# Optimization experiments

Hardware: AMD Instinct MI355X
Metric: run time of the kernel (lower is better)

## Reference

```python
import math
import jax, jax.numpy as jnp
import numpy as np

PATCH_NUMS = (1, 2, 3, 4, 5, 6, 8, 10, 13, 16)
_lens = [p * p for p in PATCH_NUMS]
_cum = np.concatenate([[0], np.cumsum(_lens)])
BEGIN_ENDS = [(int(_cum[i]), int(_cum[i + 1])) for i in range(len(PATCH_NUMS))]
L_TOTAL = int(_cum[-1])  # 680

B, C = 32, 1024
S, P, M, R, NCAT = 10, 8, 4, 8, 22
SLOTS = P * M  # 32 slots per scale
MEM_RANK = 64
ALPHA_HID = 128


def setup_inputs() -> dict:
    key = jax.random.key(0)
    ks = jax.random.split(key, 24)
    inp = {}
    inp['x'] = jax.random.normal(ks[0], (B, L_TOTAL, C), jnp.float32)
    # -1 means CFG-unconditional sample (no category memory)
    inp['category_ids'] = jax.random.randint(ks[1], (B,), -1, NCAT)
    # shared memory, orthogonal-ish init rescaled to xavier std sqrt(2/(C+C))
    inp['shared_memory'] = jax.random.normal(ks[2], (S, SLOTS, C)) * math.sqrt(1.0 / C)
    inp['cat_A'] = jax.random.normal(ks[3], (NCAT, S, R)) * 0.01
    inp['cat_B'] = jax.random.normal(ks[4], (S, R, SLOTS * C)) * (1.0 / math.sqrt(R))
    inp['cat_emb'] = jax.random.normal(ks[5], (NCAT, C)) * 0.02
    inp['scale_emb'] = jax.random.normal(ks[6], (S, C)) * 0.02
    inp['Wq'] = jax.random.normal(ks[7], (C, C)) * (1.0 / math.sqrt(C))
    inp['Wk'] = jax.random.normal(ks[8], (C, C)) * (1.0 / math.sqrt(C))
    inp['Wv'] = jax.random.normal(ks[9], (C, C)) * (1.0 / math.sqrt(C))
    inp['aW1'] = jax.random.normal(ks[10], (3 * C, ALPHA_HID)) * (1.0 / math.sqrt(3 * C))
    inp['ab1'] = jnp.zeros((ALPHA_HID,), jnp.float32)
    inp['aW2'] = jax.random.normal(ks[11], (ALPHA_HID, 1)) * 0.01  # init zeros in torch; small random to exercise math
    inp['ab2'] = jnp.full((1,), -1.0, jnp.float32)
    inp['kW1'] = jax.random.normal(ks[12], (C, MEM_RANK)) * (1.0 / math.sqrt(C))
    inp['kb1'] = jnp.zeros((MEM_RANK,), jnp.float32)
    inp['kW2'] = jax.random.normal(ks[13], (MEM_RANK, C)) * (1.0 / math.sqrt(MEM_RANK))
    inp['kb2'] = jnp.zeros((C,), jnp.float32)
    inp['vW1'] = jax.random.normal(ks[14], (C, MEM_RANK)) * (1.0 / math.sqrt(C))
    inp['vb1'] = jnp.zeros((MEM_RANK,), jnp.float32)
    inp['vW2'] = jax.random.normal(ks[15], (MEM_RANK, C)) * (1.0 / math.sqrt(MEM_RANK))
    inp['vb2'] = jnp.zeros((C,), jnp.float32)
    inp['gk_logit'] = jnp.float32(-2.0)  # block_idx=0, depth=16
    inp['gv_logit'] = jnp.float32(-2.0)
    inp['log_temp'] = jnp.float32(math.log(0.1))
    return inp


def reference(x, category_ids, shared_memory, cat_A, cat_B, cat_emb, scale_emb,
              Wq, Wk, Wv, aW1, ab1, aW2, ab2,
              kW1, kb1, kW2, kb2, vW1, vb1, vW2, vb2,
              gk_logit, gv_logit, log_temp):
    Bb, L, Cc = x.shape
    temp = jnp.clip(jnp.exp(log_temp), 0.05, 1.0)
    inv_sqrt_c = 1.0 / math.sqrt(Cc)

    query = x @ Wq                              # [B, L, C]
    shared_k = shared_memory @ Wk               # [S, slots, C]
    shared_v = shared_memory @ Wv

    valid = (category_ids >= 0)                 # [B]
    cid = jnp.clip(category_ids, 0, None)
    a_all = cat_A[cid]                          # [B, S, R]
    ce = cat_emb[cid]                           # [B, C]

    outs = []
    for i, (s, e) in enumerate(BEGIN_ENDS):
        q = query[:, s:e, :]                    # [B, Ls, C]
        Ls = e - s
        V = i + 1                               # visible scales
        # --- shared retrieval over visible slots ---
        ks_ = shared_k[:V].reshape(V * SLOTS, Cc)
        vs_ = shared_v[:V].reshape(V * SLOTS, Cc)
        attn_s = jax.nn.softmax((q @ ks_.T) * inv_sqrt_c / temp, axis=-1)
        o_s = attn_s @ vs_                      # [B, Ls, C]
        # --- per-category memory: shared + low-rank residual ---
        delta = jnp.einsum('bvr,vrd->bvd', a_all[:, :V], cat_B[:V])
        delta = delta.reshape(Bb, V, SLOTS, Cc)
        cat_mem = (shared_memory[:V][None] + delta).reshape(Bb, V * SLOTS, Cc)
        kc = cat_mem @ Wk                       # [B, Vs, C]
        vc = cat_mem @ Wv
        attn_c = jax.nn.softmax(jnp.einsum('bld,bsd->bls', q, kc) * inv_sqrt_c / temp, axis=-1)
        o_c = jnp.einsum('bls,bsd->bld', attn_c, vc)
        # --- learned alpha blend (zeroed for invalid / CFG categories) ---
        ai = jnp.concatenate([
            q,
            jnp.broadcast_to(ce[:, None, :], (Bb, Ls, Cc)),
            jnp.broadcast_to(scale_emb[i][None, None, :], (Bb, Ls, Cc)),
        ], axis=-1)                             # [B, Ls, 3C]
        h = jax.nn.gelu(ai @ aW1 + ab1, approximate=False)
        alpha = jax.nn.sigmoid(h @ aW2 + ab2)   # [B, Ls, 1]
        alpha = jnp.where(valid[:, None, None], alpha, 0.0)
        outs.append(o_s + alpha * (o_c - o_s))

    mem = jnp.concatenate(outs, axis=1)         # [B, L, C]
    mem_k = jax.nn.sigmoid(gk_logit) * ((mem @ kW1 + kb1) @ kW2 + kb2)
    mem_v = jax.nn.sigmoid(gv_logit) * ((mem @ vW1 + vb1) @ vW2 + vb2)
    zero = jnp.float32(0.0)
    return mem_k, mem_v, zero, zero
```

## Files before the change

### kernel.cpp

```cpp
#include <hip/hip_runtime.h>
#include <math.h>

#define NB 32
#define NC 1024
#define LTOT 680

typedef unsigned short u16;
typedef __bf16 bf16x8 __attribute__((ext_vector_type(8)));
typedef float floatx4 __attribute__((ext_vector_type(4)));

__device__ __forceinline__ u16 f2bf(float f)
{
    union { float f; unsigned u; } v; v.f = f;
    unsigned u = v.u;
    u += 0x7FFFu + ((u >> 16) & 1u);
    return (u16)(u >> 16);
}

__device__ __forceinline__ float bf2f(unsigned u)
{
    union { unsigned u; float f; } v; v.u = u << 16; return v.f;
}

template<int AFP32, int OUTBF>
__global__ __launch_bounds__(256) void gemm_mfma(
    const void* __restrict__ Av, const u16* __restrict__ BT,
    float* __restrict__ C, int M, int N, int K, int lda,
    const float* __restrict__ bias, const float* __restrict__ scale_logit)
{
    __shared__ __align__(16) u16 As[16 * 64 * 8];
    __shared__ __align__(16) u16 Bs[16 * 64 * 8];

    const int tid  = threadIdx.x;
    const int m0   = blockIdx.x << 7;
    const int n0   = blockIdx.y << 7;
    const int wave = tid >> 6;
    const int lane = tid & 63;
    const int mh   = wave & 1;
    const int nh   = wave >> 1;

    floatx4 acc[4][4];
#pragma unroll
    for (int i = 0; i < 4; ++i)
#pragma unroll
        for (int j = 0; j < 4; ++j) acc[i][j] = (floatx4){0.f, 0.f, 0.f, 0.f};

    for (int k0 = 0; k0 < K; k0 += 64) {
        __syncthreads();
        if (AFP32) {
            const float* A = (const float*)Av;
#pragma unroll
            for (int p = 0; p < 8; ++p) {
                int q   = tid + (p << 8);
                int row = q >> 4;
                int fq  = q & 15;
                int gr  = m0 + row; if (gr > M - 1) gr = M - 1;
                const float4 a4 = *(const float4*)(A + (size_t)gr * lda + k0 + (fq << 2));
                int kh = fq >> 3, quad = (fq >> 1) & 3, jh = fq & 1;
                u16* d = &As[((((row >> 4) << 1) | kh) * 64 + (quad << 4) + (row & 15)) * 8 + (jh << 2)];
                d[0] = f2bf(a4.x); d[1] = f2bf(a4.y); d[2] = f2bf(a4.z); d[3] = f2bf(a4.w);
            }
        } else {
            const u16* A = (const u16*)Av;
#pragma unroll
            for (int p = 0; p < 4; ++p) {
                int q   = tid + (p << 8);
                int row = q >> 3;
                int cq  = q & 7;
                int gr  = m0 + row; if (gr > M - 1) gr = M - 1;
                *(uint4*)&As[((((row >> 4) << 1) | (cq >> 2)) * 64 + ((cq & 3) << 4) + (row & 15)) * 8]
                    = *(const uint4*)(A + (size_t)gr * lda + k0 + (cq << 3));
            }
        }
#pragma unroll
        for (int p = 0; p < 4; ++p) {
            int q   = tid + (p << 8);
            int row = q >> 3;
            int cq  = q & 7;
            int gn  = n0 + row; if (gn > N - 1) gn = N - 1;
            *(uint4*)&Bs[((((row >> 4) << 1) | (cq >> 2)) * 64 + ((cq & 3) << 4) + (row & 15)) * 8]
                = *(const uint4*)(BT + (size_t)gn * K + k0 + (cq << 3));
        }
        __syncthreads();
#pragma unroll
        for (int kh = 0; kh < 2; ++kh) {
            bf16x8 a[4], b[4];
#pragma unroll
            for (int i = 0; i < 4; ++i)
                a[i] = *(const bf16x8*)&As[(((((mh << 2) + i) << 1) | kh) * 64 + lane) * 8];
#pragma unroll
            for (int j = 0; j < 4; ++j)
                b[j] = *(const bf16x8*)&Bs[(((((nh << 2) + j) << 1) | kh) * 64 + lane) * 8];
#pragma unroll
            for (int i = 0; i < 4; ++i)
#pragma unroll
                for (int j = 0; j < 4; ++j)
                    acc[i][j] = __builtin_amdgcn_mfma_f32_16x16x32_bf16(a[i], b[j], acc[i][j], 0, 0, 0);
        }
    }

    float scale = 1.f;
    if (scale_logit) scale = 1.f / (1.f + __expf(-scale_logit[0]));
    const int col = lane & 15, rquad = lane >> 4;
#pragma unroll
    for (int i = 0; i < 4; ++i) {
#pragma unroll
        for (int j = 0; j < 4; ++j) {
#pragma unroll
            for (int r = 0; r < 4; ++r) {
                int gr = m0 + (mh << 6) + (i << 4) + (rquad << 2) + r;
                int gc = n0 + (nh << 6) + (j << 4) + col;
                if (gr < M && gc < N) {
                    float bb = bias ? bias[gc] : 0.f;
                    float val = scale * (acc[i][j][r] + bb);
                    if (OUTBF) ((u16*)C)[(size_t)gr * N + gc] = f2bf(val);
                    else       C[(size_t)gr * N + gc] = val;
                }
            }
        }
    }
}

__global__ __launch_bounds__(256) void gemm_logits(
    const u16* __restrict__ Q, const u16* __restrict__ skb,
    const u16* __restrict__ kcb, float* __restrict__ out)
{
    __shared__ __align__(16) u16 As[16 * 64 * 8];
    __shared__ __align__(16) u16 Bs[16 * 64 * 8];

    const int tid  = threadIdx.x;
    const int m0   = blockIdx.x << 7;
    const int n0   = blockIdx.y << 7;
    const int b    = blockIdx.z;
    const int wave = tid >> 6;
    const int lane = tid & 63;
    const int mh   = wave & 1;
    const int nh   = wave >> 1;

    const u16* Ab = Q   + (size_t)b * 680 * 1024;
    const u16* KC = kcb + (size_t)b * 320 * 1024;

    floatx4 acc[4][4];
#pragma unroll
    for (int i = 0; i < 4; ++i)
#pragma unroll
        for (int j = 0; j < 4; ++j) acc[i][j] = (floatx4){0.f, 0.f, 0.f, 0.f};

    for (int k0 = 0; k0 < 1024; k0 += 64) {
        __syncthreads();
#pragma unroll
        for (int p = 0; p < 4; ++p) {
            int q = tid + (p << 8);
            int row = q >> 3, cq = q & 7;
            int gr = m0 + row; if (gr > 679) gr = 679;
            *(uint4*)&As[((((row >> 4) << 1) | (cq >> 2)) * 64 + ((cq & 3) << 4) + (row & 15)) * 8]
                = *(const uint4*)(Ab + (size_t)gr * 1024 + k0 + (cq << 3));
        }
#pragma unroll
        for (int p = 0; p < 4; ++p) {
            int q = tid + (p << 8);
            int row = q >> 3, cq = q & 7;
            int gn = n0 + row;
            const u16* src = (gn < 320) ? (skb + (size_t)gn * 1024)
                                        : (KC + (size_t)(gn - 320) * 1024);
            *(uint4*)&Bs[((((row >> 4) << 1) | (cq >> 2)) * 64 + ((cq & 3) << 4) + (row & 15)) * 8]
                = *(const uint4*)(src + k0 + (cq << 3));
        }
        __syncthreads();
#pragma unroll
        for (int kh = 0; kh < 2; ++kh) {
            bf16x8 a[4], bb[4];
#pragma unroll
            for (int i = 0; i < 4; ++i)
                a[i] = *(const bf16x8*)&As[(((((mh << 2) + i) << 1) | kh) * 64 + lane) * 8];
#pragma unroll
            for (int j = 0; j < 4; ++j)
                bb[j] = *(const bf16x8*)&Bs[(((((nh << 2) + j) << 1) | kh) * 64 + lane) * 8];
#pragma unroll
            for (int i = 0; i < 4; ++i)
#pragma unroll
                for (int j = 0; j < 4; ++j)
                    acc[i][j] = __builtin_amdgcn_mfma_f32_16x16x32_bf16(a[i], bb[j], acc[i][j], 0, 0, 0);
        }
    }

    const int col = lane & 15, rquad = lane >> 4;
#pragma unroll
    for (int i = 0; i < 4; ++i)
#pragma unroll
        for (int j = 0; j < 4; ++j)
#pragma unroll
            for (int r = 0; r < 4; ++r) {
                int gr = m0 + (mh << 6) + (i << 4) + (rquad << 2) + r;
                int gc = n0 + (nh << 6) + (j << 4) + col;
                if (gr < 680)
                    out[((size_t)b * 680 + gr) * 640 + gc] = acc[i][j][r];
            }
}

__global__ __launch_bounds__(256) void gemm_pv(
    const u16* __restrict__ P, const u16* __restrict__ svT,
    const u16* __restrict__ vcT, float* __restrict__ out)
{
    __shared__ __align__(16) u16 As[16 * 64 * 8];
    __shared__ __align__(16) u16 Bs[16 * 64 * 8];

    const int tid  = threadIdx.x;
    const int m0   = blockIdx.x << 7;
    const int n0   = blockIdx.y << 7;
    const int b    = blockIdx.z;
    const int wave = tid >> 6;
    const int lane = tid & 63;
    const int mh   = wave & 1;
    const int nh   = wave >> 1;

    floatx4 acc[4][4];
#pragma unroll
    for (int i = 0; i < 4; ++i)
#pragma unroll
        for (int j = 0; j < 4; ++j) acc[i][j] = (floatx4){0.f, 0.f, 0.f, 0.f};

    for (int k0 = 0; k0 < 640; k0 += 64) {
        __syncthreads();
#pragma unroll
        for (int p = 0; p < 4; ++p) {
            int q = tid + (p << 8);
            int row = q >> 3, cq = q & 7;
            int gr = m0 + row; if (gr > 679) gr = 679;
            *(uint4*)&As[((((row >> 4) << 1) | (cq >> 2)) * 64 + ((cq & 3) << 4) + (row & 15)) * 8]
                = *(const uint4*)(P + ((size_t)b * 680 + gr) * 1280 + k0 + (cq << 3));
        }
#pragma unroll
        for (int p = 0; p < 4; ++p) {
            int q = tid + (p << 8);
            int row = q >> 3, cq = q & 7;
            int gn = n0 + row;
            const u16* src = (k0 < 320)
                ? (svT + (size_t)gn * 320 + k0)
                : (vcT + ((size_t)b * 1024 + gn) * 320 + (k0 - 320));
            *(uint4*)&Bs[((((row >> 4) << 1) | (cq >> 2)) * 64 + ((cq & 3) << 4) + (row & 15)) * 8]
                = *(const uint4*)(src + (cq << 3));
        }
        __syncthreads();
#pragma unroll
        for (int kh = 0; kh < 2; ++kh) {
            bf16x8 a[4], bb[4];
#pragma unroll
            for (int i = 0; i < 4; ++i)
                a[i] = *(const bf16x8*)&As[(((((mh << 2) + i) << 1) | kh) * 64 + lane) * 8];
#pragma unroll
            for (int j = 0; j < 4; ++j)
                bb[j] = *(const bf16x8*)&Bs[(((((nh << 2) + j) << 1) | kh) * 64 + lane) * 8];
#pragma unroll
            for (int i = 0; i < 4; ++i)
#pragma unroll
                for (int j = 0; j < 4; ++j)
                    acc[i][j] = __builtin_amdgcn_mfma_f32_16x16x32_bf16(a[i], bb[j], acc[i][j], 0, 0, 0);
        }
    }

    const int col = lane & 15, rquad = lane >> 4;
#pragma unroll
    for (int i = 0; i < 4; ++i)
#pragma unroll
        for (int j = 0; j < 4; ++j)
#pragma unroll
            for (int r = 0; r < 4; ++r) {
                int gr = m0 + (mh << 6) + (i << 4) + (rquad << 2) + r;
                int gc = n0 + (nh << 6) + (j << 4) + col;
                if (gr < 680)
                    out[((size_t)b * 680 + gr) * 1024 + gc] = acc[i][j][r];
            }
}

__global__ __launch_bounds__(256) void gemm_halpha(
    const u16* __restrict__ Q, const u16* __restrict__ W,
    const float* __restrict__ ceW, const float* __restrict__ seW,
    const int* __restrict__ cat_ids, u16* __restrict__ h)
{
    __shared__ __align__(16) u16 As[16 * 64 * 8];
    __shared__ __align__(16) u16 Bs[16 * 64 * 8];

    const int tid  = threadIdx.x;
    const int m0   = blockIdx.x << 7;
    const int wave = tid >> 6;
    const int lane = tid & 63;
    const int mh   = wave & 1;
    const int nh   = wave >> 1;

    floatx4 acc[4][4];
#pragma unroll
    for (int i = 0; i < 4; ++i)
#pragma unroll
        for (int j = 0; j < 4; ++j) acc[i][j] = (floatx4){0.f, 0.f, 0.f, 0.f};

    for (int k0 = 0; k0 < 1024; k0 += 64) {
        __syncthreads();
#pragma unroll
        for (int p = 0; p < 4; ++p) {
            int q = tid + (p << 8);
            int row = q >> 3, cq = q & 7;
            int gr = m0 + row;
            *(uint4*)&As[((((row >> 4) << 1) | (cq >> 2)) * 64 + ((cq & 3) << 4) + (row & 15)) * 8]
                = *(const uint4*)(Q + (size_t)gr * 1024 + k0 + (cq << 3));
        }
#pragma unroll
        for (int p = 0; p < 4; ++p) {
            int q = tid + (p << 8);
            int row = q >> 3, cq = q & 7;
            *(uint4*)&Bs[((((row >> 4) << 1) | (cq >> 2)) * 64 + ((cq & 3) << 4) + (row & 15)) * 8]
                = *(const uint4*)(W + (size_t)row * 1024 + k0 + (cq << 3));
        }
        __syncthreads();
#pragma unroll
        for (int kh = 0; kh < 2; ++kh) {
            bf16x8 a[4], bb[4];
#pragma unroll
            for (int i = 0; i < 4; ++i)
                a[i] = *(const bf16x8*)&As[(((((mh << 2) + i) << 1) | kh) * 64 + lane) * 8];
#pragma unroll
            for (int j = 0; j < 4; ++j)
                bb[j] = *(const bf16x8*)&Bs[(((((nh << 2) + j) << 1) | kh) * 64 + lane) * 8];
#pragma unroll
            for (int i = 0; i < 4; ++i)
#pragma unroll
                for (int j = 0; j < 4; ++j)
                    acc[i][j] = __builtin_amdgcn_mfma_f32_16x16x32_bf16(a[i], bb[j], acc[i][j], 0, 0, 0);
        }
    }

    const int se_[9] = {1,5,14,30,55,91,155,255,424};
    const int col = lane & 15, rquad = lane >> 4;
#pragma unroll
    for (int i = 0; i < 4; ++i) {
#pragma unroll
        for (int r = 0; r < 4; ++r) {
            int gr = m0 + (mh << 6) + (i << 4) + (rquad << 2) + r;
            int b  = gr / 680;
            int l  = gr - b * 680;
            int isc = 0;
#pragma unroll
            for (int k = 0; k < 9; ++k) if (l >= se_[k]) isc = k + 1;
            int cid = cat_ids[b]; if (cid < 0) cid = 0;
            const float* cw = ceW + cid * 128;
            const float* sw = seW + isc * 128;
#pragma unroll
            for (int j = 0; j < 4; ++j) {
                int gc = (nh << 6) + (j << 4) + col;
                float val = acc[i][j][r] + cw[gc] + sw[gc];
                float g = 0.5f * val * (1.0f + erff(val * 0.70710678118654752f));
                h[(size_t)gr * 128 + gc] = f2bf(g);
            }
        }
    }
}

__global__ __launch_bounds__(256) void alpha_reduce(
    const u16* __restrict__ h, const float* __restrict__ aW2,
    const float* __restrict__ ab2, const int* __restrict__ cat_ids,
    float* __restrict__ alpha)
{
    const int wave = threadIdx.x >> 6;
    const int lane = threadIdx.x & 63;
    const int row  = (blockIdx.x << 2) + wave;

    const unsigned pk = *(const unsigned*)(h + (size_t)row * 128 + (lane << 1));
    float s = bf2f(pk) * aW2[lane << 1] + bf2f(pk >> 16) * aW2[(lane << 1) + 1];
#pragma unroll
    for (int k = 32; k >= 1; k >>= 1) s += __shfl_xor(s, k);
    if (lane == 0) {
        int b = row / 680;
        float al = 0.f;
        if (cat_ids[b] >= 0) al = 1.f / (1.f + expf(-(s + ab2[0])));
        alpha[row] = al;
    }
}

__global__ __launch_bounds__(256) void softmax_kernel(
    float* __restrict__ logits, const float* __restrict__ alpha,
    const float* __restrict__ log_temp)
{
    const int tid  = threadIdx.x;
    const int w    = tid >> 6;
    const int lane = tid & 63;
    const int b    = blockIdx.y;
    const int l    = (blockIdx.x << 2) + w;

    const int se[10] = {1,5,14,30,55,91,155,255,424,680};
    int isc = 0;
#pragma unroll
    for (int k = 0; k < 9; ++k) if (l >= se[k]) isc = k + 1;
    const int NK = (isc + 1) << 5;

    float temp = __expf(log_temp[0]);
    temp = fminf(fmaxf(temp, 0.05f), 1.0f);
    const float Ksc = 0.03125f / temp;

    float* row = logits + ((size_t)b * 680 + l) * 640;

    float ls[5], lc[5];
#pragma unroll
    for (int u = 0; u < 5; ++u) {
        int j = lane + (u << 6);
        bool v = j < NK;
        ls[u] = v ? row[j]       : -1e30f;
        lc[u] = v ? row[320 + j] : -1e30f;
    }
    float mxs = -1e30f, mxc = -1e30f;
#pragma unroll
    for (int u = 0; u < 5; ++u) { mxs = fmaxf(mxs, ls[u]); mxc = fmaxf(mxc, lc[u]); }
#pragma unroll
    for (int k = 32; k >= 1; k >>= 1) {
        mxs = fmaxf(mxs, __shfl_xor(mxs, k));
        mxc = fmaxf(mxc, __shfl_xor(mxc, k));
    }
    float es[5], ec[5], ss = 0.f, sc = 0.f;
#pragma unroll
    for (int u = 0; u < 5; ++u) {
        int j = lane + (u << 6);
        bool v = j < NK;
        es[u] = v ? __expf((ls[u] - mxs) * Ksc) : 0.f;
        ec[u] = v ? __expf((lc[u] - mxc) * Ksc) : 0.f;
        ss += es[u]; sc += ec[u];
    }
#pragma unroll
    for (int k = 32; k >= 1; k >>= 1) {
        ss += __shfl_xor(ss, k);
        sc += __shfl_xor(sc, k);
    }
    const float al = alpha[b * LTOT + l];
    const float wS = (1.f - al) / ss;
    const float wC = al / sc;

    u16* po = (u16*)row;
#pragma unroll
    for (int u = 0; u < 5; ++u) {
        int j = lane + (u << 6);
        po[j]       = f2bf(es[u] * wS);
        po[320 + j] = f2bf(ec[u] * wC);
    }
}

__global__ __launch_bounds__(256) void castbf(
    const float* __restrict__ in, u16* __restrict__ out, int n4)
{
    int i = blockIdx.x * 256 + threadIdx.x;
    const int stride = gridDim.x * 256;
    for (; i < n4; i += stride) {
        const float4 v = ((const float4*)in)[i];
        uint2 o;
        o.x = (unsigned)f2bf(v.x) | ((unsigned)f2bf(v.y) << 16);
        o.y = (unsigned)f2bf(v.z) | ((unsigned)f2bf(v.w) << 16);
        ((uint2*)out)[i] = o;
    }
}

__global__ __launch_bounds__(256) void tcast(
    const float* __restrict__ in, u16* __restrict__ out, int R, int Cc)
{
    __shared__ float t[32][33];
    const int bx = blockIdx.x * 32;
    const int by = blockIdx.y * 32;
    const int x = threadIdx.x & 31;
    const int y0 = threadIdx.x >> 5;
#pragma unroll
    for (int yy = y0; yy < 32; yy += 8)
        t[yy][x] = (by + yy < R && bx + x < Cc)
                 ? in[(size_t)(by + yy) * Cc + bx + x] : 0.f;
    __syncthreads();
#pragma unroll
    for (int yy = y0; yy < 32; yy += 8)
        if (bx + yy < Cc && by + x < R)
            out[(size_t)(bx + yy) * R + by + x] = f2bf(t[x][yy]);
}

__global__ __launch_bounds__(256) void transpose32(
    const float* __restrict__ in, float* __restrict__ out, int R, int Cc)
{
    __shared__ float t[32][33];
    const int bx = blockIdx.x * 32;
    const int by = blockIdx.y * 32;
    const int x = threadIdx.x & 31;
    const int y0 = threadIdx.x >> 5;
#pragma unroll
    for (int yy = y0; yy < 32; yy += 8)
        t[yy][x] = (by + yy < R && bx + x < Cc)
                 ? in[(size_t)(by + yy) * Cc + bx + x] : 0.f;
    __syncthreads();
#pragma unroll
    for (int yy = y0; yy < 32; yy += 8)
        if (bx + yy < Cc && by + x < R)
            out[(size_t)(bx + yy) * R + by + x] = t[x][yy];
}

__global__ __launch_bounds__(256) void build_kc(
    const float* __restrict__ sk, const float* __restrict__ catBK,
    const float* __restrict__ cat_A, const int* __restrict__ cat_ids,
    u16* __restrict__ kc)
{
    const int b = blockIdx.x;
    const int jrow = blockIdx.y;
    const int v = jrow >> 5, slot = jrow & 31;
    int cid = cat_ids[b]; if (cid < 0) cid = 0;
    float a[8];
#pragma unroll
    for (int r = 0; r < 8; ++r) a[r] = cat_A[(cid * 10 + v) * 8 + r];
    const int c = threadIdx.x << 2;
    float4 acc = *(const float4*)(sk + (size_t)jrow * 1024 + c);
#pragma unroll
    for (int r = 0; r < 8; ++r) {
        const float4 bv = *(const float4*)(catBK + (size_t)((v * 8 + r) * 32 + slot) * 1024 + c);
        acc.x = fmaf(a[r], bv.x, acc.x);
        acc.y = fmaf(a[r], bv.y, acc.y);
        acc.z = fmaf(a[r], bv.z, acc.z);
        acc.w = fmaf(a[r], bv.w, acc.w);
    }
    uint2 pk;
    pk.x = (unsigned)f2bf(acc.x) | ((unsigned)f2bf(acc.y) << 16);
    pk.y = (unsigned)f2bf(acc.z) | ((unsigned)f2bf(acc.w) << 16);
    *(uint2*)(kc + ((size_t)b * 320 + jrow) * 1024 + c) = pk;
}

__global__ __launch_bounds__(320) void build_vcT(
    const float* __restrict__ svT, const float* __restrict__ catBVT,
    const float* __restrict__ cat_A, const int* __restrict__ cat_ids,
    u16* __restrict__ vcT)
{
    __shared__ float aS[80];
    const int b = blockIdx.x;
    const int c = blockIdx.y;
    const int tid = threadIdx.x;
    if (tid < 80) {
        int cid = cat_ids[b]; if (cid < 0) cid = 0;
        aS[tid] = cat_A[cid * 80 + tid];
    }
    __syncthreads();
    const int j = tid;
    const int v = j >> 5, slot = j & 31;
    float acc = svT[(size_t)c * 320 + j];
    const float* row = catBVT + (size_t)c * 2560;
#pragma unroll
    for (int r = 0; r < 8; ++r)
        acc = fmaf(aS[v * 8 + r], row[(v * 8 + r) * 32 + slot], acc);
    vcT[((size_t)b * 1024 + c) * 320 + j] = f2bf(acc);
}

__global__ void concat_bias(const float* __restrict__ a,
                            const float* __restrict__ b, float* __restrict__ o)
{
    int t = threadIdx.x;
    if (t < 64) o[t] = a[t];
    else if (t < 128) o[t] = b[t - 64];
}

__global__ void tail_zero(float* p)
{
    if (threadIdx.x < 2) p[threadIdx.x] = 0.f;
}

extern "C" void kernel_launch(void* const* d_in, const int* in_sizes, int n_in,
                              void* d_out, int out_size, void* d_ws, size_t ws_size,
                              hipStream_t stream)
{
    (void)in_sizes; (void)n_in;
    const float* x         = (const float*)d_in[0];
    const int*   cat_ids   = (const int*)  d_in[1];
    const float* sm        = (const float*)d_in[2];
    const float* cat_A     = (const float*)d_in[3];
    const float* cat_B     = (const float*)d_in[4];
    const float* cat_emb   = (const float*)d_in[5];
    const float* scale_emb = (const float*)d_in[6];
    const float* Wq        = (const float*)d_in[7];
    const float* Wk        = (const float*)d_in[8];
    const float* Wv        = (const float*)d_in[9];
    const float* aW1       = (const float*)d_in[10];
    const float* ab1       = (const float*)d_in[11];
    const float* aW2       = (const float*)d_in[12];
    const float* ab2       = (const float*)d_in[13];
    const float* kW1       = (const float*)d_in[14];
    const float* kb1       = (const float*)d_in[15];
    const float* kW2       = (const float*)d_in[16];
    const float* kb2       = (const float*)d_in[17];
    const float* vW1       = (const float*)d_in[18];
    const float* vb1       = (const float*)d_in[19];
    const float* vW2       = (const float*)d_in[20];
    const float* vb2       = (const float*)d_in[21];
    const float* gk        = (const float*)d_in[22];
    const float* gv        = (const float*)d_in[23];
    const float* log_temp  = (const float*)d_in[24];

    float* out   = (float*)d_out;
    float* memb  = out;
    float* outv  = out + (size_t)21760 * 1024;

    float* w      = (float*)d_ws;
    u16*   kc_bf  = (u16*)w;
    u16*   vcT_bf = (u16*)(w + 5242880);
    float* sk     = w + 10485760;
    float* sv     = w + 10813440;
    float* svT    = w + 11141120;
    u16*   sk_bf  = (u16*)(w + 11468800);
    u16*   svT_bf = (u16*)(w + 11632640);
    float* alph   = w + 11796480;
    float* logits = w + 11859200;
    float* tail0  = w + 25785600;
    u16*   aW1topT = (u16*)tail0;
    u16*   aW1midT = (u16*)(tail0 + 65536);
    u16*   aW1botT = (u16*)(tail0 + 131072);
    float* ceW    = tail0 + 196608;
    float* seW    = tail0 + 199424;
    float* cb     = tail0 + 200704;
    u16*   h_bf   = (u16*)(tail0 + 200832);
    if (ws_size < (size_t)29881600 * 4) return;
    if (out_size < 2 * 21760 * 1024 + 2) return;

    u16*   x_bf   = (u16*)logits;
    float* bufA   = logits + 5570560;
    float* bufB   = bufA + 2621440;
    float* catBVT = bufB + 2621440;
    u16*   WqT    = (u16*)w;
    u16*   WkT    = WqT + 1048576;
    u16*   WvT    = WkT + 1048576;
    u16*   kW1T   = (u16*)sv;
    u16*   vW1T   = kW1T + 65536;
    u16*   kW2T   = vW1T + 65536;
    u16*   vW2T   = kW2T + 65536;
    float* bufAB  = w;
    u16*   query_bf = (u16*)outv;

    const dim3 blk256(256);

    castbf<<<dim3(2048), blk256, 0, stream>>>(x, x_bf, 21760 * 1024 / 4);
    tcast<<<dim3(32, 32), blk256, 0, stream>>>(Wq, WqT, 1024, 1024);
    tcast<<<dim3(32, 32), blk256, 0, stream>>>(Wk, WkT, 1024, 1024);
    tcast<<<dim3(32, 32), blk256, 0, stream>>>(Wv, WvT, 1024, 1024);
    tcast<<<dim3(4, 32), blk256, 0, stream>>>(aW1,              aW1topT, 1024, 128);
    tcast<<<dim3(4, 32), blk256, 0, stream>>>(aW1 + 1024 * 128, aW1midT, 1024, 128);
    tcast<<<dim3(4, 32), blk256, 0, stream>>>(aW1 + 2048 * 128, aW1botT, 1024, 128);

    gemm_mfma<0,1><<<dim3(170, 8), blk256, 0, stream>>>(x_bf, WqT, (float*)query_bf, 21760, 1024, 1024, 1024, nullptr, nullptr);
    gemm_mfma<1,0><<<dim3(3, 8),   blk256, 0, stream>>>(sm,   WkT, sk,   320,  1024, 1024, 1024, nullptr, nullptr);
    gemm_mfma<1,0><<<dim3(3, 8),   blk256, 0, stream>>>(sm,   WvT, sv,   320,  1024, 1024, 1024, nullptr, nullptr);
    gemm_mfma<1,0><<<dim3(20, 8),  blk256, 0, stream>>>(cat_B, WkT, bufA, 2560, 1024, 1024, 1024, nullptr, nullptr);
    gemm_mfma<1,0><<<dim3(20, 8),  blk256, 0, stream>>>(cat_B, WvT, bufB, 2560, 1024, 1024, 1024, nullptr, nullptr);

    gemm_mfma<1,0><<<dim3(1, 1), blk256, 0, stream>>>(cat_emb,   aW1midT, ceW, 22, 128, 1024, 1024, nullptr, nullptr);
    gemm_mfma<1,0><<<dim3(1, 1), blk256, 0, stream>>>(scale_emb, aW1botT, seW, 10, 128, 1024, 1024, ab1, nullptr);

    castbf<<<dim3(320), blk256, 0, stream>>>(sk, sk_bf, 320 * 1024 / 4);
    transpose32<<<dim3(32, 10), blk256, 0, stream>>>(sv, svT, 320, 1024);
    tcast<<<dim3(32, 10), blk256, 0, stream>>>(sv, svT_bf, 320, 1024);
    transpose32<<<dim3(32, 80), blk256, 0, stream>>>(bufB, catBVT, 2560, 1024);
    tcast<<<dim3(2, 32), blk256, 0, stream>>>(kW1, kW1T, 1024, 64);
    tcast<<<dim3(2, 32), blk256, 0, stream>>>(vW1, vW1T, 1024, 64);
    tcast<<<dim3(32, 2), blk256, 0, stream>>>(kW2, kW2T, 64, 1024);
    tcast<<<dim3(32, 2), blk256, 0, stream>>>(vW2, vW2T, 64, 1024);
    concat_bias<<<dim3(1), dim3(128), 0, stream>>>(kb1, vb1, cb);

    build_kc<<<dim3(NB, 320), blk256, 0, stream>>>(sk, bufA, cat_A, cat_ids, kc_bf);
    build_vcT<<<dim3(NB, 1024), dim3(320), 0, stream>>>(svT, catBVT, cat_A, cat_ids, vcT_bf);

    gemm_halpha<<<dim3(170), blk256, 0, stream>>>(query_bf, aW1topT, ceW, seW, cat_ids, h_bf);
    alpha_reduce<<<dim3(5440), blk256, 0, stream>>>(h_bf, aW2, ab2, cat_ids, alph);

    gemm_logits<<<dim3(6, 5, NB), blk256, 0, stream>>>(query_bf, sk_bf, kc_bf, logits);
    softmax_kernel<<<dim3(170, NB), blk256, 0, stream>>>(logits, alph, log_temp);
    gemm_pv<<<dim3(6, 8, NB), blk256, 0, stream>>>((const u16*)logits, svT_bf, vcT_bf, memb);

    gemm_mfma<1,0><<<dim3(170, 1), blk256, 0, stream>>>(memb, kW1T, bufAB, 21760, 128, 1024, 1024, cb, nullptr);
    gemm_mfma<1,0><<<dim3(170, 8), blk256, 0, stream>>>(bufAB,      kW2T, memb, 21760, 1024, 64, 128, kb2, gk);
    gemm_mfma<1,0><<<dim3(170, 8), blk256, 0, stream>>>(bufAB + 64, vW2T, outv, 21760, 1024, 64, 128, vb2, gv);

    tail_zero<<<1, 64, 0, stream>>>(out + (size_t)2 * 21760 * 1024);
}
```

Baseline: 1.101 ms.

## Use direct global-to-LDS loads and bf16 intermediates across GEMM kernels

Swaps register-staged global loads into shared memory for the gfx9 global_load_lds path in every bf16 GEMM kernel, with per-thread source pointers precomputed once. To make more GEMMs take the bf16 path, it pre-casts shared_memory and cat_B to bf16 and makes the PV output and low-rank intermediate bf16 instead of fp32. It also swaps the grid axes so N tiles vary fastest, improving reuse of A tiles in cache. This cuts LDS store instructions and fp32 traffic, at the cost of extra cast kernels and reduced precision in intermediates.

```diff
diff --git a/kernel.cpp b/kernel.cpp
--- a/kernel.cpp
+++ b/kernel.cpp
@@ -20,6 +20,22 @@
 __device__ __forceinline__ float bf2f(unsigned u)
 {
     union { unsigned u; float f; } v; v.u = u << 16; return v.f;
+}
+
+__device__ __forceinline__ void gload16(const u16* g, u16* l)
+{
+    typedef __attribute__((address_space(1))) const void gv_t;
+    typedef __attribute__((address_space(3))) void lv_t;
+    __builtin_amdgcn_global_load_lds(
+        (gv_t*)(unsigned long long)(const void*)g,
+        (lv_t*)(unsigned int)(unsigned long long)(void*)l,
+        16, 0, 0);
+}
+
+__device__ __forceinline__ void slot_decode(int s, int* prow, int* pcq)
+{
+    *prow = ((s >> 7) << 4) | (s & 15);
+    *pcq  = (((s >> 6) & 1) << 2) | ((s >> 4) & 3);
 }
 
 template<int AFP32, int OUTBF>
@@ -32,12 +48,27 @@
     __shared__ __align__(16) u16 Bs[16 * 64 * 8];
 
     const int tid  = threadIdx.x;
-    const int m0   = blockIdx.x << 7;
-    const int n0   = blockIdx.y << 7;
+    const int m0   = blockIdx.y << 7;
+    const int n0   = blockIdx.x << 7;
     const int wave = tid >> 6;
     const int lane = tid & 63;
     const int mh   = wave & 1;
     const int nh   = wave >> 1;
+
+    const u16* aSrc[4];
+    const u16* bSrc[4];
+#pragma unroll
+    for (int p = 0; p < 4; ++p) {
+        int s, row, cq;
+        s = tid + (p << 8);
+        slot_decode(s, &row, &cq);
+        if (!AFP32) {
+            int gr = m0 + row; if (gr > M - 1) gr = M - 1;
+            aSrc[p] = (const u16*)Av + (size_t)gr * lda + (cq << 3);
+        }
+        int gn = n0 + row; if (gn > N - 1) gn = N - 1;
+        bSrc[p] = BT + (size_t)gn * K + (cq << 3);
+    }
 
     floatx4 acc[4][4];
 #pragma unroll
@@ -61,26 +92,13 @@
                 d[0] = f2bf(a4.x); d[1] = f2bf(a4.y); d[2] = f2bf(a4.z); d[3] = f2bf(a4.w);
             }
         } else {
-            const u16* A = (const u16*)Av;
-#pragma unroll
-            for (int p = 0; p < 4; ++p) {
-                int q   = tid + (p << 8);
-                int row = q >> 3;
-                int cq  = q & 7;
-                int gr  = m0 + row; if (gr > M - 1) gr = M - 1;
-                *(uint4*)&As[((((row >> 4) << 1) | (cq >> 2)) * 64 + ((cq & 3) << 4) + (row & 15)) * 8]
-                    = *(const uint4*)(A + (size_t)gr * lda + k0 + (cq << 3));
-            }
-        }
-#pragma unroll
-        for (int p = 0; p < 4; ++p) {
-            int q   = tid + (p << 8);
-            int row = q >> 3;
-            int cq  = q & 7;
-            int gn  = n0 + row; if (gn > N - 1) gn = N - 1;
-            *(uint4*)&Bs[((((row >> 4) << 1) | (cq >> 2)) * 64 + ((cq & 3) << 4) + (row & 15)) * 8]
-                = *(const uint4*)(BT + (size_t)gn * K + k0 + (cq << 3));
-        }
+#pragma unroll
+            for (int p = 0; p < 4; ++p)
+                gload16(aSrc[p] + k0, As + ((wave << 6) + (p << 8)) * 8);
+        }
+#pragma unroll
+        for (int p = 0; p < 4; ++p)
+            gload16(bSrc[p] + k0, Bs + ((wave << 6) + (p << 8)) * 8);
         __syncthreads();
 #pragma unroll
         for (int kh = 0; kh < 2; ++kh) {
@@ -140,6 +158,20 @@
     const u16* Ab = Q   + (size_t)b * 680 * 1024;
     const u16* KC = kcb + (size_t)b * 320 * 1024;
 
+    const u16* aSrc[4];
+    const u16* bSrc[4];
+#pragma unroll
+    for (int p = 0; p < 4; ++p) {
+        int s, row, cq;
+        s = tid + (p << 8);
+        slot_decode(s, &row, &cq);
+        int gr = m0 + row; if (gr > 679) gr = 679;
+        aSrc[p] = Ab + (size_t)gr * 1024 + (cq << 3);
+        int gn = n0 + row;
+        bSrc[p] = ((gn < 320) ? (skb + (size_t)gn * 1024)
+                              : (KC + (size_t)(gn - 320) * 1024)) + (cq << 3);
+    }
+
     floatx4 acc[4][4];
 #pragma unroll
     for (int i = 0; i < 4; ++i)
@@ -149,23 +181,11 @@
     for (int k0 = 0; k0 < 1024; k0 += 64) {
         __syncthreads();
 #pragma unroll
-        for (int p = 0; p < 4; ++p) {
-            int q = tid + (p << 8);
-            int row = q >> 3, cq = q & 7;
-            int gr = m0 + row; if (gr > 679) gr = 679;
-            *(uint4*)&As[((((row >> 4) << 1) | (cq >> 2)) * 64 + ((cq & 3) << 4) + (row & 15)) * 8]
-                = *(const uint4*)(Ab + (size_t)gr * 1024 + k0 + (cq << 3));
-        }
-#pragma unroll
-        for (int p = 0; p < 4; ++p) {
-            int q = tid + (p << 8);
-            int row = q >> 3, cq = q & 7;
-            int gn = n0 + row;
-            const u16* src = (gn < 320) ? (skb + (size_t)gn * 1024)
-                                        : (KC + (size_t)(gn - 320) * 1024);
-            *(uint4*)&Bs[((((row >> 4) << 1) | (cq >> 2)) * 64 + ((cq & 3) << 4) + (row & 15)) * 8]
-                = *(const uint4*)(src + k0 + (cq << 3));
-        }
+        for (int p = 0; p < 4; ++p)
+            gload16(aSrc[p] + k0, As + ((wave << 6) + (p << 8)) * 8);
+#pragma unroll
+        for (int p = 0; p < 4; ++p)
+            gload16(bSrc[p] + k0, Bs + ((wave << 6) + (p << 8)) * 8);
         __syncthreads();
 #pragma unroll
         for (int kh = 0; kh < 2; ++kh) {
@@ -200,7 +220,7 @@
 
 __global__ __launch_bounds__(256) void gemm_pv(
     const u16* __restrict__ P, const u16* __restrict__ svT,
-    const u16* __restrict__ vcT, float* __restrict__ out)
+    const u16* __restrict__ vcT, u16* __restrict__ out)
 {
     __shared__ __align__(16) u16 As[16 * 64 * 8];
     __shared__ __align__(16) u16 Bs[16 * 64 * 8];
@@ -214,6 +234,21 @@
     const int mh   = wave & 1;
     const int nh   = wave >> 1;
 
+    const u16* aSrc[4];
+    const u16* bSrcS[4];
+    const u16* bSrcC[4];
+#pragma unroll
+    for (int p = 0; p < 4; ++p) {
+        int s, row, cq;
+        s = tid + (p << 8);
+        slot_decode(s, &row, &cq);
+        int gr = m0 + row; if (gr > 679) gr = 679;
+        aSrc[p] = P + ((size_t)b * 680 + gr) * 1280 + (cq << 3);
+        int gn = n0 + row;
+        bSrcS[p] = svT + (size_t)gn * 320 + (cq << 3);
+        bSrcC[p] = vcT + ((size_t)b * 1024 + gn) * 320 + (cq << 3);
+    }
+
     floatx4 acc[4][4];
 #pragma unroll
     for (int i = 0; i < 4; ++i)
@@ -223,23 +258,12 @@
     for (int k0 = 0; k0 < 640; k0 += 64) {
         __syncthreads();
 #pragma unroll
+        for (int p = 0; p < 4; ++p)
+            gload16(aSrc[p] + k0, As + ((wave << 6) + (p << 8)) * 8);
+#pragma unroll
         for (int p = 0; p < 4; ++p) {
-            int q = tid + (p << 8);
-            int row = q >> 3, cq = q & 7;
-            int gr = m0 + row; if (gr > 679) gr = 679;
-            *(uint4*)&As[((((row >> 4) << 1) | (cq >> 2)) * 64 + ((cq & 3) << 4) + (row & 15)) * 8]
-                = *(const uint4*)(P + ((size_t)b * 680 + gr) * 1280 + k0 + (cq << 3));
-        }
-#pragma unroll
-        for (int p = 0; p < 4; ++p) {
-            int q = tid + (p << 8);
-            int row = q >> 3, cq = q & 7;
-            int gn = n0 + row;
-            const u16* src = (k0 < 320)
-                ? (svT + (size_t)gn * 320 + k0)
-                : (vcT + ((size_t)b * 1024 + gn) * 320 + (k0 - 320));
-            *(uint4*)&Bs[((((row >> 4) << 1) | (cq >> 2)) * 64 + ((cq & 3) << 4) + (row & 15)) * 8]
-                = *(const uint4*)(src + (cq << 3));
+            const u16* bp = (k0 < 320) ? (bSrcS[p] + k0) : (bSrcC[p] + (k0 - 320));
+            gload16(bp, Bs + ((wave << 6) + (p << 8)) * 8);
         }
         __syncthreads();
 #pragma unroll
@@ -269,7 +293,7 @@
                 int gr = m0 + (mh << 6) + (i << 4) + (rquad << 2) + r;
                 int gc = n0 + (nh << 6) + (j << 4) + col;
                 if (gr < 680)
-                    out[((size_t)b * 680 + gr) * 1024 + gc] = acc[i][j][r];
+                    out[((size_t)b * 680 + gr) * 1024 + gc] = f2bf(acc[i][j][r]);
             }
 }
 
@@ -288,6 +312,17 @@
     const int mh   = wave & 1;
     const int nh   = wave >> 1;
 
+    const u16* aSrc[4];
+    const u16* bSrc[4];
+#pragma unroll
+    for (int p = 0; p < 4; ++p) {
+        int s, row, cq;
+        s = tid + (p << 8);
+        slot_decode(s, &row, &cq);
+        aSrc[p] = Q + (size_t)(m0 + row) * 1024 + (cq << 3);
+        bSrc[p] = W + (size_t)row * 1024 + (cq << 3);
+    }
+
     floatx4 acc[4][4];
 #pragma unroll
     for (int i = 0; i < 4; ++i)
@@ -297,20 +332,11 @@
     for (int k0 = 0; k0 < 1024; k0 += 64) {
         __syncthreads();
 #pragma unroll
-        for (int p = 0; p < 4; ++p) {
-            int q = tid + (p << 8);
-            int row = q >> 3, cq = q & 7;
-            int gr = m0 + row;
-            *(uint4*)&As[((((row >> 4) << 1) | (cq >> 2)) * 64 + ((cq & 3) << 4) + (row & 15)) * 8]
-                = *(const uint4*)(Q + (size_t)gr * 1024 + k0 + (cq << 3));
-        }
-#pragma unroll
-        for (int p = 0; p < 4; ++p) {
-            int q = tid + (p << 8);
-            int row = q >> 3, cq = q & 7;
-            *(uint4*)&Bs[((((row >> 4) << 1) | (cq >> 2)) * 64 + ((cq & 3) << 4) + (row & 15)) * 8]
-                = *(const uint4*)(W + (size_t)row * 1024 + k0 + (cq << 3));
-        }
+        for (int p = 0; p < 4; ++p)
+            gload16(aSrc[p] + k0, As + ((wave << 6) + (p << 8)) * 8);
+#pragma unroll
+        for (int p = 0; p < 4; ++p)
+            gload16(bSrc[p] + k0, Bs + ((wave << 6) + (p << 8)) * 8);
         __syncthreads();
 #pragma unroll
         for (int kh = 0; kh < 2; ++kh) {
@@ -611,6 +637,8 @@
     float* seW    = tail0 + 199424;
     float* cb     = tail0 + 200704;
     u16*   h_bf   = (u16*)(tail0 + 200832);
+    u16*   catB_bf = (u16*)(w + 27379072);
+    u16*   sm_bf  = (u16*)(w + 28689792);
     if (ws_size < (size_t)29881600 * 4) return;
     if (out_size < 2 * 21760 * 1024 + 2) return;
 
@@ -625,12 +653,15 @@
     u16*   vW1T   = kW1T + 65536;
     u16*   kW2T   = vW1T + 65536;
     u16*   vW2T   = kW2T + 65536;
-    float* bufAB  = w;
+    u16*   bufAB_bf = (u16*)w;
+    u16*   mem_bf = (u16*)memb;
     u16*   query_bf = (u16*)outv;
 
     const dim3 blk256(256);
 
     castbf<<<dim3(2048), blk256, 0, stream>>>(x, x_bf, 21760 * 1024 / 4);
+    castbf<<<dim3(320), blk256, 0, stream>>>(sm, sm_bf, 320 * 1024 / 4);
+    castbf<<<dim3(2048), blk256, 0, stream>>>(cat_B, catB_bf, 2560 * 1024 / 4);
     tcast<<<dim3(32, 32), blk256, 0, stream>>>(Wq, WqT, 1024, 1024);
     tcast<<<dim3(32, 32), blk256, 0, stream>>>(Wk, WkT, 1024, 1024);
     tcast<<<dim3(32, 32), blk256, 0, stream>>>(Wv, WvT, 1024, 1024);
@@ -638,11 +669,11 @@
     tcast<<<dim3(4, 32), blk256, 0, stream>>>(aW1 + 1024 * 128, aW1midT, 1024, 128);
     tcast<<<dim3(4, 32), blk256, 0, stream>>>(aW1 + 2048 * 128, aW1botT, 1024, 128);
 
-    gemm_mfma<0,1><<<dim3(170, 8), blk256, 0, stream>>>(x_bf, WqT, (float*)query_bf, 21760, 1024, 1024, 1024, nullptr, nullptr);
-    gemm_mfma<1,0><<<dim3(3, 8),   blk256, 0, stream>>>(sm,   WkT, sk,   320,  1024, 1024, 1024, nullptr, nullptr);
-    gemm_mfma<1,0><<<dim3(3, 8),   blk256, 0, stream>>>(sm,   WvT, sv,   320,  1024, 1024, 1024, nullptr, nullptr);
-    gemm_mfma<1,0><<<dim3(20, 8),  blk256, 0, stream>>>(cat_B, WkT, bufA, 2560, 1024, 1024, 1024, nullptr, nullptr);
-    gemm_mfma<1,0><<<dim3(20, 8),  blk256, 0, stream>>>(cat_B, WvT, bufB, 2560, 1024, 1024, 1024, nullptr, nullptr);
+    gemm_mfma<0,1><<<dim3(8, 170), blk256, 0, stream>>>(x_bf,    WqT, (float*)query_bf, 21760, 1024, 1024, 1024, nullptr, nullptr);
+    gemm_mfma<0,0><<<dim3(8, 3),   blk256, 0, stream>>>(sm_bf,   WkT, sk,   320,  1024, 1024, 1024, nullptr, nullptr);
+    gemm_mfma<0,0><<<dim3(8, 3),   blk256, 0, stream>>>(sm_bf,   WvT, sv,   320,  1024, 1024, 1024, nullptr, nullptr);
+    gemm_mfma<0,0><<<dim3(8, 20),  blk256, 0, stream>>>(catB_bf, WkT, bufA, 2560, 1024, 1024, 1024, nullptr, nullptr);
+    gemm_mfma<0,0><<<dim3(8, 20),  blk256, 0, stream>>>(catB_bf, WvT, bufB, 2560, 1024, 1024, 1024, nullptr, nullptr);
 
     gemm_mfma<1,0><<<dim3(1, 1), blk256, 0, stream>>>(cat_emb,   aW1midT, ceW, 22, 128, 1024, 1024, nullptr, nullptr);
     gemm_mfma<1,0><<<dim3(1, 1), blk256, 0, stream>>>(scale_emb, aW1botT, seW, 10, 128, 1024, 1024, ab1, nullptr);
@@ -665,11 +696,11 @@
 
     gemm_logits<<<dim3(6, 5, NB), blk256, 0, stream>>>(query_bf, sk_bf, kc_bf, logits);
     softmax_kernel<<<dim3(170, NB), blk256, 0, stream>>>(logits, alph, log_temp);
-    gemm_pv<<<dim3(6, 8, NB), blk256, 0, stream>>>((const u16*)logits, svT_bf, vcT_bf, memb);
-
-    gemm_mfma<1,0><<<dim3(170, 1), blk256, 0, stream>>>(memb, kW1T, bufAB, 21760, 128, 1024, 1024, cb, nullptr);
-    gemm_mfma<1,0><<<dim3(170, 8), blk256, 0, stream>>>(bufAB,      kW2T, memb, 21760, 1024, 64, 128, kb2, gk);
-    gemm_mfma<1,0><<<dim3(170, 8), blk256, 0, stream>>>(bufAB + 64, vW2T, outv, 21760, 1024, 64, 128, vb2, gv);
+    gemm_pv<<<dim3(6, 8, NB), blk256, 0, stream>>>((const u16*)logits, svT_bf, vcT_bf, mem_bf);
+
+    gemm_mfma<0,1><<<dim3(1, 170), blk256, 0, stream>>>(mem_bf, kW1T, (float*)bufAB_bf, 21760, 128, 1024, 1024, cb, nullptr);
+    gemm_mfma<0,0><<<dim3(8, 170), blk256, 0, stream>>>(bufAB_bf,      kW2T, memb, 21760, 1024, 64, 128, kb2, gk);
+    gemm_mfma<0,0><<<dim3(8, 170), blk256, 0, stream>>>(bufAB_bf + 64, vW2T, outv, 21760, 1024, 64, 128, vb2, gv);
 
     tail_zero<<<1, 64, 0, stream>>>(out + (size_t)2 * 21760 * 1024);
 }
```

Measured after the change: 1.046 ms. -5.0%, faster.
